# Optimization experiments

Measured on AMD Instinct MI355X. Metric: run time of the kernel, lower is better.

The kernel has to match this reference:

```python
import jax, jax.numpy as jnp
import numpy as np

FP16_HUGE = 65504.0  # large additive mask constant (fp16-max style, as in AF2 torch ports)

B, N, T = 1, 384, 4
CQ, CT = 128, 64      # query (pair) channels, template pair channels
H = 4                 # num heads
D = CT // H           # per-head key/value dim = 16 (AF2: key_dim=value_dim=64 split over 4 heads)


def setup_inputs() -> dict:
    key = jax.random.key(0)
    ks = jax.random.split(key, 8)
    inp = {
        "query_embedding": jax.random.normal(ks[0], (B, N, N, CQ), jnp.float32),
        "template_pair_representation": jax.random.normal(ks[1], (B, T, N, N, CT), jnp.float32),
        "template_mask": jnp.ones((B, T), jnp.float32),
        # attention params (gating=False for template pointwise attention in AF2)
        "query_w": jax.random.normal(ks[2], (H, CQ, D), jnp.float32) * (CQ ** -0.5),
        "key_w": jax.random.normal(ks[3], (H, CT, D), jnp.float32) * (CT ** -0.5),
        "value_w": jax.random.normal(ks[4], (H, CT, D), jnp.float32) * (CT ** -0.5),
        "output_w": jax.random.normal(ks[5], (H, D, CQ), jnp.float32) * ((H * D) ** -0.5),
        "output_b": jnp.zeros((CQ,), jnp.float32),
    }
    return inp


def reference(query_embedding, template_pair_representation, template_mask,
              query_w, key_w, value_w, output_w, output_b):
    b, n, _, cq = query_embedding.shape
    t = template_mask.shape[-1]
    d = query_w.shape[-1]

    # [b, n*n, 1, cq]: each (i,j) pair position attends over templates
    flat_q = query_embedding.reshape(b, n * n, 1, cq)
    # [b, t, n, n, ct] -> [b, n, n, t, ct] -> [b, n*n, t, ct]
    flat_t = jnp.transpose(template_pair_representation, (0, 2, 3, 1, 4)).reshape(b, n * n, t, -1)

    # additive bias over key axis: 0 where mask=1, -FP16_HUGE where mask=0; [b,1,1,1,t]
    bias = FP16_HUGE * (template_mask[:, None, None, None, :] - 1.0)

    q = jnp.einsum('bpic,hcd->bphid', flat_q, query_w) * (d ** -0.5)  # [b,p,h,1,d]
    k = jnp.einsum('bptc,hcd->bphtd', flat_t, key_w)                  # [b,p,h,t,d]
    v = jnp.einsum('bptc,hcd->bphtd', flat_t, value_w)

    logits = jnp.einsum('bphid,bphtd->bphit', q, k) + bias            # [b,p,h,1,t]
    weights = jax.nn.softmax(logits, axis=-1)
    wv = jnp.einsum('bphit,bphtd->bphid', weights, v)                 # [b,p,h,1,d]
    out = jnp.einsum('bphid,hdc->bpic', wv, output_w) + output_b      # [b,p,1,cq]

    embedding = out.reshape(b, n, n, cq)
    tmask = (jnp.sum(template_mask.reshape(b, -1), axis=1) > 0.0).astype(embedding.dtype)
    return embedding * tmask[:, None, None, None]
```

## Files before the change

kernel.cpp:

```cpp
#include <hip/hip_runtime.h>
#include <hip/hip_bf16.h>

typedef __attribute__((ext_vector_type(8))) short bf16x8;
typedef __attribute__((ext_vector_type(4))) float f32x4;
typedef unsigned int u32;
typedef unsigned short u16;

#define NPOS 147456
#define NTILES 9216
#define NBLK 768
#define ITERS 12

__device__ inline u16 bfc(float f) {
  union { __hip_bfloat16 h; u16 s; } u;
  u.h = __float2bfloat16(f);
  return u.s;
}

__global__ void prep_kernel(const float* __restrict__ wq, const float* __restrict__ wk,
                            const float* __restrict__ wv, const float* __restrict__ wo,
                            u16* __restrict__ wsf) {
  int gid = blockIdx.x * 256 + threadIdx.x;
  int idx, which;
  if (gid < 8192)       { idx = gid;         which = 0; }
  else if (gid < 12288) { idx = gid - 8192;  which = 1; }
  else if (gid < 16384) { idx = gid - 12288; which = 2; }
  else                  { idx = gid - 16384; which = 3; }
  int fragid = idx >> 9, lane = (idx >> 3) & 63, e = idx & 7;
  int l15 = lane & 15, g = lane >> 4;
  float v;
  if (which == 0) {
    int n = fragid >> 2, kc = fragid & 3;
    int c = kc * 32 + g * 8 + e;
    v = wq[n * 2048 + c * 16 + l15] * 0.25f;
  } else if (which == 1) {
    int n = fragid >> 1, kc = fragid & 1;
    int c = kc * 32 + g * 8 + e;
    v = wk[n * 1024 + c * 16 + l15];
  } else if (which == 2) {
    int n = fragid >> 1, kc = fragid & 1;
    int c = kc * 32 + g * 8 + e;
    v = wv[n * 1024 + c * 16 + l15];
  } else {
    int n8 = fragid >> 1, kc = fragid & 1;
    int hd = kc * 32 + g * 8 + e;
    v = wo[(hd >> 4) * 2048 + (hd & 15) * 128 + n8 * 16 + l15];
  }
  wsf[gid] = bfc(v);
}

#define WQF(n, kc)  ((((n) * 4 + (kc))) * 64)
#define WKF(n, kc)  ((16 + (n) * 2 + (kc)) * 64)
#define WVF(n, kc)  ((24 + (n) * 2 + (kc)) * 64)
#define WOF(n8, kc) ((32 + (n8) * 2 + (kc)) * 64)

typedef const __attribute__((address_space(1))) u32 gas_u32;
typedef __attribute__((address_space(3))) u32 las_u32;

__global__ __launch_bounds__(256) void tpa_kernel(
    const float* __restrict__ qe, const float* __restrict__ tpr,
    const float* __restrict__ tmk_p, const float* __restrict__ ob,
    const u16* __restrict__ wsf, float* __restrict__ out)
{
  __shared__ int4 inbuf4[2][1536];
  __shared__ u32 wvsh32[512];
  char* const inb0 = (char*)inbuf4[0];
  char* const inb1 = (char*)inbuf4[1];
  char* const wvsh = (char*)wvsh32;

  const int tid = threadIdx.x;
  const int wid = tid >> 6;
  const int lane = tid & 63;
  const int l15 = lane & 15, g = lane >> 4;
  const int swz = (l15 & 7) << 4;
  const int h = wid;

  const char* dmab[6]; int dmstr[6];
  #pragma unroll
  for (int j = 0; j < 6; ++j) {
    int k = wid + 4 * j, m = k * 64 + lane;
    if (m < 512) {
      int pos = m >> 5, inner = ((m & 31) * 16) ^ ((pos & 7) << 4);
      dmab[j] = (const char*)qe + (size_t)pos * 512 + inner; dmstr[j] = 512;
    } else {
      int m2 = m - 512, t = m2 >> 8, pos = (m2 >> 4) & 15;
      int inner = ((m2 & 15) * 16) ^ ((pos & 7) << 4);
      dmab[j] = (const char*)tpr + ((size_t)t * NPOS + pos) * 256 + inner; dmstr[j] = 256;
    }
  }

#define STAGE(DST, P)                                                          \
  { _Pragma("unroll") for (int j = 0; j < 6; ++j) {                            \
      const char* s_ = dmab[j] + (size_t)(P) * dmstr[j];                       \
      char* d_ = (DST) + (wid + 4 * j) * 1024;                                 \
      __builtin_amdgcn_global_load_lds((gas_u32*)s_, (las_u32*)d_, 16, 0, 0); } }

  STAGE(inb0, blockIdx.x * 16)

  const bf16x8* wf = (const bf16x8*)wsf;
  bf16x8 wqf[4], wkf[2], wvf[2], wof[2][2];
  #pragma unroll
  for (int kc = 0; kc < 4; ++kc) wqf[kc] = wf[WQF(h, kc) + lane];
  #pragma unroll
  for (int kc = 0; kc < 2; ++kc) {
    wkf[kc] = wf[WKF(h, kc) + lane];
    wvf[kc] = wf[WVF(h, kc) + lane];
    wof[0][kc] = wf[WOF(2 * h + 0, kc) + lane];
    wof[1][kc] = wf[WOF(2 * h + 1, kc) + lane];
  }

  const float m0 = tmk_p[0], m1 = tmk_p[1], m2 = tmk_p[2], m3 = tmk_p[3];
  const float biasv[4] = {65504.0f * (m0 - 1.0f), 65504.0f * (m1 - 1.0f),
                          65504.0f * (m2 - 1.0f), 65504.0f * (m3 - 1.0f)};
  const float tmk = (m0 + m1 + m2 + m3 > 0.0f) ? 1.0f : 0.0f;

  f32x4 obf[2];
  {
    const f32x4* obase = reinterpret_cast<const f32x4*>(ob);
    #pragma unroll
    for (int j = 0; j < 2; ++j) {
      const f32x4 o = obase[(2 * h + j) * 4 + g];
      #pragma unroll
      for (int r = 0; r < 4; ++r) obf[j][r] = o[r] * tmk;
    }
  }

  STAGE(inb1, (blockIdx.x + NBLK) * 16)

#define BODY(IT, CB)                                                           \
{                                                                              \
  const int p0 = (blockIdx.x + (IT) * NBLK) * 16;                              \
  __builtin_amdgcn_sched_barrier(0);                                           \
  asm volatile("s_waitcnt vmcnt(6)" ::: "memory");                             \
  __builtin_amdgcn_s_barrier();                                                \
  __builtin_amdgcn_sched_barrier(0);                                           \
  const char* qrow = (CB) + l15 * 512;                                         \
  f32x4 qT = (f32x4){0.f, 0.f, 0.f, 0.f};                                      \
  _Pragma("unroll")                                                            \
  for (int kc = 0; kc < 4; ++kc) {                                             \
    const int cb = kc * 128 + g * 32;                                          \
    f32x4 lo = *(const f32x4*)(qrow + ((cb) ^ swz));                           \
    f32x4 hi = *(const f32x4*)(qrow + ((cb + 16) ^ swz));                      \
    bf16x8 aq;                                                                 \
    _Pragma("unroll")                                                          \
    for (int e = 0; e < 4; ++e) { aq[e] = (short)bfc(lo[e]); aq[e + 4] = (short)bfc(hi[e]); } \
    qT = __builtin_amdgcn_mfma_f32_16x16x32_bf16(wqf[kc], aq, qT, 0, 0, 0);    \
  }                                                                            \
  float ssum = 0.f;                                                            \
  f32x4 wvT = (f32x4){0.f, 0.f, 0.f, 0.f};                                     \
  _Pragma("unroll")                                                            \
  for (int t = 0; t < 4; ++t) {                                                \
    const char* trow = (CB) + 8192 + t * 4096 + l15 * 256;                     \
    bf16x8 at0, at1;                                                           \
    { f32x4 lo = *(const f32x4*)(trow + ((g * 32) ^ swz));                     \
      f32x4 hi = *(const f32x4*)(trow + ((g * 32 + 16) ^ swz));                \
      _Pragma("unroll")                                                        \
      for (int e = 0; e < 4; ++e) { at0[e] = (short)bfc(lo[e]); at0[e + 4] = (short)bfc(hi[e]); } } \
    { f32x4 lo = *(const f32x4*)(trow + ((128 + g * 32) ^ swz));               \
      f32x4 hi = *(const f32x4*)(trow + ((128 + g * 32 + 16) ^ swz));          \
      _Pragma("unroll")                                                        \
      for (int e = 0; e < 4; ++e) { at1[e] = (short)bfc(lo[e]); at1[e + 4] = (short)bfc(hi[e]); } } \
    f32x4 kT = (f32x4){0.f, 0.f, 0.f, 0.f};                                    \
    f32x4 vT = (f32x4){0.f, 0.f, 0.f, 0.f};                                    \
    kT = __builtin_amdgcn_mfma_f32_16x16x32_bf16(wkf[0], at0, kT, 0, 0, 0);    \
    kT = __builtin_amdgcn_mfma_f32_16x16x32_bf16(wkf[1], at1, kT, 0, 0, 0);    \
    vT = __builtin_amdgcn_mfma_f32_16x16x32_bf16(wvf[0], at0, vT, 0, 0, 0);    \
    vT = __builtin_amdgcn_mfma_f32_16x16x32_bf16(wvf[1], at1, vT, 0, 0, 0);    \
    float lg = qT[0] * kT[0] + qT[1] * kT[1] + qT[2] * kT[2] + qT[3] * kT[3];  \
    lg += __shfl_xor(lg, 16);                                                  \
    lg += __shfl_xor(lg, 32);                                                  \
    const float w = __expf(lg + biasv[t]);                                     \
    ssum += w;                                                                 \
    _Pragma("unroll")                                                          \
    for (int r = 0; r < 4; ++r) wvT[r] += w * vT[r];                           \
  }                                                                            \
  { const float inv = tmk / fmaxf(ssum, 1e-30f);                               \
    u32 pk0 = (u32)bfc(wvT[0] * inv) | ((u32)bfc(wvT[1] * inv) << 16);         \
    u32 pk1 = (u32)bfc(wvT[2] * inv) | ((u32)bfc(wvT[3] * inv) << 16);         \
    const int hb = h * 32 + g * 8;                                             \
    *(u32*)(wvsh + ((l15 * 128 + hb) ^ swz))     = pk0;                        \
    *(u32*)(wvsh + ((l15 * 128 + hb + 4) ^ swz)) = pk1; }                      \
  __builtin_amdgcn_sched_barrier(0);                                           \
  asm volatile("s_waitcnt lgkmcnt(0)" ::: "memory");                           \
  __builtin_amdgcn_s_barrier();                                                \
  __builtin_amdgcn_sched_barrier(0);                                           \
  bf16x8 bwv0 = *(const bf16x8*)(wvsh + ((l15 * 128 + g * 16)      ^ swz));    \
  bf16x8 bwv1 = *(const bf16x8*)(wvsh + ((l15 * 128 + 64 + g * 16) ^ swz));    \
  _Pragma("unroll")                                                            \
  for (int j = 0; j < 2; ++j) {                                                \
    f32x4 acc = (f32x4){0.f, 0.f, 0.f, 0.f};                                   \
    acc = __builtin_amdgcn_mfma_f32_16x16x32_bf16(wof[j][0], bwv0, acc, 0, 0, 0); \
    acc = __builtin_amdgcn_mfma_f32_16x16x32_bf16(wof[j][1], bwv1, acc, 0, 0, 0); \
    f32x4 res;                                                                 \
    _Pragma("unroll")                                                          \
    for (int r = 0; r < 4; ++r) res[r] = acc[r] + obf[j][r];                   \
    *(f32x4*)(out + (size_t)(p0 + l15) * 128 + (2 * h + j) * 16 + g * 4) = res; \
  }                                                                            \
  __builtin_amdgcn_sched_barrier(0);                                           \
  { const int sit = ((IT) + 2 < ITERS) ? (IT) + 2 : (IT);                      \
    STAGE(CB, (blockIdx.x + sit * NBLK) * 16) }                                \
}

  for (int ith = 0; ith < ITERS / 2; ++ith) {
    BODY(2 * ith,     inb0)
    BODY(2 * ith + 1, inb1)
  }
}

extern "C" void kernel_launch(void* const* d_in, const int* in_sizes, int n_in,
                              void* d_out, int out_size, void* d_ws, size_t ws_size,
                              hipStream_t stream) {
  const float* qe  = (const float*)d_in[0];
  const float* tpr = (const float*)d_in[1];
  const float* tmk = (const float*)d_in[2];
  const float* wq  = (const float*)d_in[3];
  const float* wk  = (const float*)d_in[4];
  const float* wv  = (const float*)d_in[5];
  const float* wo  = (const float*)d_in[6];
  const float* ob  = (const float*)d_in[7];
  float* out = (float*)d_out;
  u16* wsf = (u16*)d_ws;

  prep_kernel<<<96, 256, 0, stream>>>(wq, wk, wv, wo, wsf);
  tpa_kernel<<<NBLK, 256, 0, stream>>>(qe, tpr, tmk, ob, wsf, out);
}
```

Measured before the change: 64.44 us.

## Load query rows straight to registers and issue template DMA earlier

Query-embedding rows are now loaded from global memory straight into registers, one iteration ahead, instead of going through the LDS DMA staging buffer. Only template-pair data is staged via global_load_lds, so the double buffer shrinks and the vmcnt wait thresholds are recomputed for the new load counts. The next-tile stage and query prefetch are issued right after the second barrier, before the output MFMAs and stores, to overlap more. A launch-bounds occupancy hint of 2 blocks is added, which trades register headroom for the extra live query registers against potential spilling.

```diff
diff --git a/kernel.cpp b/kernel.cpp
--- a/kernel.cpp
+++ b/kernel.cpp
@@ -57,12 +57,15 @@
 typedef const __attribute__((address_space(1))) u32 gas_u32;
 typedef __attribute__((address_space(3))) u32 las_u32;
 
-__global__ __launch_bounds__(256) void tpa_kernel(
+#define STR2_(x) #x
+#define WAITVM(n) asm volatile("s_waitcnt vmcnt(" STR2_(n) ")" ::: "memory")
+
+__global__ __launch_bounds__(256, 2) void tpa_kernel(
     const float* __restrict__ qe, const float* __restrict__ tpr,
     const float* __restrict__ tmk_p, const float* __restrict__ ob,
     const u16* __restrict__ wsf, float* __restrict__ out)
 {
-  __shared__ int4 inbuf4[2][1536];
+  __shared__ int4 inbuf4[2][1024];
   __shared__ u32 wvsh32[512];
   char* const inb0 = (char*)inbuf4[0];
   char* const inb1 = (char*)inbuf4[1];
@@ -75,27 +78,28 @@
   const int swz = (l15 & 7) << 4;
   const int h = wid;
 
-  const char* dmab[6]; int dmstr[6];
+  const char* dmab[4];
   #pragma unroll
-  for (int j = 0; j < 6; ++j) {
-    int k = wid + 4 * j, m = k * 64 + lane;
-    if (m < 512) {
-      int pos = m >> 5, inner = ((m & 31) * 16) ^ ((pos & 7) << 4);
-      dmab[j] = (const char*)qe + (size_t)pos * 512 + inner; dmstr[j] = 512;
-    } else {
-      int m2 = m - 512, t = m2 >> 8, pos = (m2 >> 4) & 15;
-      int inner = ((m2 & 15) * 16) ^ ((pos & 7) << 4);
-      dmab[j] = (const char*)tpr + ((size_t)t * NPOS + pos) * 256 + inner; dmstr[j] = 256;
-    }
+  for (int j = 0; j < 4; ++j) {
+    int m = (wid * 4 + j) * 64 + lane;
+    int t = m >> 8, pos = (m >> 4) & 15, c16 = m & 15;
+    int inner = (c16 * 16) ^ ((pos & 7) << 4);
+    dmab[j] = (const char*)tpr + ((size_t)t * NPOS + pos) * 256 + inner;
   }
 
 #define STAGE(DST, P)                                                          \
-  { _Pragma("unroll") for (int j = 0; j < 6; ++j) {                            \
-      const char* s_ = dmab[j] + (size_t)(P) * dmstr[j];                       \
-      char* d_ = (DST) + (wid + 4 * j) * 1024;                                 \
+  { _Pragma("unroll") for (int j = 0; j < 4; ++j) {                            \
+      const char* s_ = dmab[j] + (size_t)(P) * 256;                            \
+      char* d_ = (DST) + (wid * 4 + j) * 1024;                                 \
       __builtin_amdgcn_global_load_lds((gas_u32*)s_, (las_u32*)d_, 16, 0, 0); } }
 
-  STAGE(inb0, blockIdx.x * 16)
+#define LOADQ(P)                                                               \
+  { const f32x4* qb = reinterpret_cast<const f32x4*>(qe) + ((P) + l15) * 32 + g * 2; \
+    _Pragma("unroll")                                                          \
+    for (int kc = 0; kc < 4; ++kc) {                                           \
+      qv[kc * 2 + 0] = qb[kc * 8 + 0];                                         \
+      qv[kc * 2 + 1] = qb[kc * 8 + 1];                                         \
+    } }
 
   const bf16x8* wf = (const bf16x8*)wsf;
   bf16x8 wqf[4], wkf[2], wvf[2], wof[2][2];
@@ -125,32 +129,36 @@
     }
   }
 
+  f32x4 qv[8];
+  LOADQ(blockIdx.x * 16)
+  __builtin_amdgcn_sched_barrier(0);
+  STAGE(inb0, blockIdx.x * 16)
   STAGE(inb1, (blockIdx.x + NBLK) * 16)
-
-#define BODY(IT, CB)                                                           \
+  __builtin_amdgcn_sched_barrier(0);
+
+#define BODY(IT, CB, WN)                                                       \
 {                                                                              \
   const int p0 = (blockIdx.x + (IT) * NBLK) * 16;                              \
   __builtin_amdgcn_sched_barrier(0);                                           \
-  asm volatile("s_waitcnt vmcnt(6)" ::: "memory");                             \
+  WAITVM(WN);                                                                  \
   __builtin_amdgcn_s_barrier();                                                \
   __builtin_amdgcn_sched_barrier(0);                                           \
-  const char* qrow = (CB) + l15 * 512;                                         \
   f32x4 qT = (f32x4){0.f, 0.f, 0.f, 0.f};                                      \
   _Pragma("unroll")                                                            \
   for (int kc = 0; kc < 4; ++kc) {                                             \
-    const int cb = kc * 128 + g * 32;                                          \
-    f32x4 lo = *(const f32x4*)(qrow + ((cb) ^ swz));                           \
-    f32x4 hi = *(const f32x4*)(qrow + ((cb + 16) ^ swz));                      \
     bf16x8 aq;                                                                 \
     _Pragma("unroll")                                                          \
-    for (int e = 0; e < 4; ++e) { aq[e] = (short)bfc(lo[e]); aq[e + 4] = (short)bfc(hi[e]); } \
+    for (int e = 0; e < 4; ++e) {                                              \
+      aq[e]     = (short)bfc(qv[kc * 2 + 0][e]);                               \
+      aq[e + 4] = (short)bfc(qv[kc * 2 + 1][e]);                               \
+    }                                                                          \
     qT = __builtin_amdgcn_mfma_f32_16x16x32_bf16(wqf[kc], aq, qT, 0, 0, 0);    \
   }                                                                            \
   float ssum = 0.f;                                                            \
   f32x4 wvT = (f32x4){0.f, 0.f, 0.f, 0.f};                                     \
   _Pragma("unroll")                                                            \
   for (int t = 0; t < 4; ++t) {                                                \
-    const char* trow = (CB) + 8192 + t * 4096 + l15 * 256;                     \
+    const char* trow = (CB) + t * 4096 + l15 * 256;                            \
     bf16x8 at0, at1;                                                           \
     { f32x4 lo = *(const f32x4*)(trow + ((g * 32) ^ swz));                     \
       f32x4 hi = *(const f32x4*)(trow + ((g * 32 + 16) ^ swz));                \
@@ -182,7 +190,13 @@
     *(u32*)(wvsh + ((l15 * 128 + hb + 4) ^ swz)) = pk1; }                      \
   __builtin_amdgcn_sched_barrier(0);                                           \
   asm volatile("s_waitcnt lgkmcnt(0)" ::: "memory");                           \
-  __builtin_amdgcn_s_barrier();                                                \
+  __builtin_amdgcn_s_barrier();                \
+  __builtin_amdgcn_sched_barrier(0);                                           \
+  { const int nqp = ((IT) + 1 < ITERS) ? (blockIdx.x + ((IT) + 1) * NBLK) * 16 : p0; \
+    LOADQ(nqp) }                                                               \
+  __builtin_amdgcn_sched_barrier(0);                                           \
+  { const int sit = ((IT) + 2 < ITERS) ? (IT) + 2 : (IT);                      \
+    STAGE(CB, (blockIdx.x + sit * NBLK) * 16) }                                \
   __builtin_amdgcn_sched_barrier(0);                                           \
   bf16x8 bwv0 = *(const bf16x8*)(wvsh + ((l15 * 128 + g * 16)      ^ swz));    \
   bf16x8 bwv1 = *(const bf16x8*)(wvsh + ((l15 * 128 + 64 + g * 16) ^ swz));    \
@@ -196,14 +210,13 @@
     for (int r = 0; r < 4; ++r) res[r] = acc[r] + obf[j][r];                   \
     *(f32x4*)(out + (size_t)(p0 + l15) * 128 + (2 * h + j) * 16 + g * 4) = res; \
   }                                                                            \
-  __builtin_amdgcn_sched_barrier(0);                                           \
-  { const int sit = ((IT) + 2 < ITERS) ? (IT) + 2 : (IT);                      \
-    STAGE(CB, (blockIdx.x + sit * NBLK) * 16) }                                \
-}
-
-  for (int ith = 0; ith < ITERS / 2; ++ith) {
-    BODY(2 * ith,     inb0)
-    BODY(2 * ith + 1, inb1)
+}
+
+  BODY(0, inb0, 4)
+  BODY(1, inb1, 14)
+  for (int ith = 1; ith < ITERS / 2; ++ith) {
+    BODY(2 * ith,     inb0, 14)
+    BODY(2 * ith + 1, inb1, 14)
   }
 }
 
@@ -214,13 +227,13 @@
   const float* tpr = (const float*)d_in[1];
   const float* tmk = (const float*)d_in[2];
   const float* wq  = (const float*)d_in[3];
+  const float* wv_ = (const float*)d_in[5];
   const float* wk  = (const float*)d_in[4];
-  const float* wv  = (const float*)d_in[5];
   const float* wo  = (const float*)d_in[6];
   const float* ob  = (const float*)d_in[7];
   float* out = (float*)d_out;
   u16* wsf = (u16*)d_ws;
 
-  prep_kernel<<<96, 256, 0, stream>>>(wq, wk, wv, wo, wsf);
+  prep_kernel<<<96, 256, 0, stream>>>(wq, wk, wv_, wo, wsf);
   tpa_kernel<<<NBLK, 256, 0, stream>>>(qe, tpr, tmk, ob, wsf, out);
 }
```

New measurement: 79.31 us. 1.23x slower.

## Split staging into half buffers and double block count for occupancy

Applied to the files above, without the earlier changes.

Replaces the two full 24KB double buffers with a single query buffer plus two template-half buffers, cutting LDS per block roughly in half. Prefetch of the next tile's query and first template half is issued mid-iteration, and the second half after the output stores. The grid grows to 1536 blocks with 6 iterations each, so more blocks can be resident per CU. The cost is more barriers per iteration and a shallower prefetch, which can expose more load latency within each block.

```diff
diff --git a/kernel.cpp b/kernel.cpp
--- a/kernel.cpp
+++ b/kernel.cpp
@@ -8,8 +8,8 @@
 
 #define NPOS 147456
 #define NTILES 9216
-#define NBLK 768
-#define ITERS 12
+#define NBLK 1536
+#define ITERS 6
 
 __device__ inline u16 bfc(float f) {
   union { __hip_bfloat16 h; u16 s; } u;
@@ -57,15 +57,24 @@
 typedef const __attribute__((address_space(1))) u32 gas_u32;
 typedef __attribute__((address_space(3))) u32 las_u32;
 
+#define STR2_(x) #x
+#define WAITVM(n) asm volatile("s_waitcnt vmcnt(" STR2_(n) ")" ::: "memory")
+#define SBAR      __builtin_amdgcn_s_barrier()
+#define SCHB      __builtin_amdgcn_sched_barrier(0)
+#define WAITLGKM  asm volatile("s_waitcnt lgkmcnt(0)" ::: "memory")
+
 __global__ __launch_bounds__(256) void tpa_kernel(
     const float* __restrict__ qe, const float* __restrict__ tpr,
     const float* __restrict__ tmk_p, const float* __restrict__ ob,
     const u16* __restrict__ wsf, float* __restrict__ out)
 {
-  __shared__ int4 inbuf4[2][1536];
+  __shared__ int4 qls4[512];
+  __shared__ int4 thA4[512];
+  __shared__ int4 thB4[512];
   __shared__ u32 wvsh32[512];
-  char* const inb0 = (char*)inbuf4[0];
-  char* const inb1 = (char*)inbuf4[1];
+  char* const qls  = (char*)qls4;
+  char* const thA  = (char*)thA4;
+  char* const thB  = (char*)thB4;
   char* const wvsh = (char*)wvsh32;
 
   const int tid = threadIdx.x;
@@ -75,27 +84,35 @@
   const int swz = (l15 & 7) << 4;
   const int h = wid;
 
-  const char* dmab[6]; int dmstr[6];
-  #pragma unroll
-  for (int j = 0; j < 6; ++j) {
-    int k = wid + 4 * j, m = k * 64 + lane;
-    if (m < 512) {
-      int pos = m >> 5, inner = ((m & 31) * 16) ^ ((pos & 7) << 4);
-      dmab[j] = (const char*)qe + (size_t)pos * 512 + inner; dmstr[j] = 512;
-    } else {
-      int m2 = m - 512, t = m2 >> 8, pos = (m2 >> 4) & 15;
-      int inner = ((m2 & 15) * 16) ^ ((pos & 7) << 4);
-      dmab[j] = (const char*)tpr + ((size_t)t * NPOS + pos) * 256 + inner; dmstr[j] = 256;
+  const char* qdb[2];
+  #pragma unroll
+  for (int j = 0; j < 2; ++j) {
+    int m = (wid * 2 + j) * 64 + lane;
+    int pos = m >> 5, c16 = m & 31;
+    qdb[j] = (const char*)qe + (size_t)pos * 512 + ((c16 * 16) ^ ((pos & 7) << 4));
+  }
+  const char* tdb[2][2];
+  #pragma unroll
+  for (int hf = 0; hf < 2; ++hf)
+    #pragma unroll
+    for (int j = 0; j < 2; ++j) {
+      int m = (wid * 2 + j) * 64 + lane;
+      int t = hf * 2 + (m >> 8), pos = (m >> 4) & 15, c16 = m & 15;
+      tdb[hf][j] = (const char*)tpr + ((size_t)t * NPOS + pos) * 256 +
+                   ((c16 * 16) ^ ((pos & 7) << 4));
     }
-  }
-
-#define STAGE(DST, P)                                                          \
-  { _Pragma("unroll") for (int j = 0; j < 6; ++j) {                            \
-      const char* s_ = dmab[j] + (size_t)(P) * dmstr[j];                       \
-      char* d_ = (DST) + (wid + 4 * j) * 1024;                                 \
+
+#define STAGE_Q(P)                                                             \
+  { _Pragma("unroll") for (int j = 0; j < 2; ++j) {                            \
+      const char* s_ = qdb[j] + (size_t)(P) * 512;                             \
+      char* d_ = qls + (wid * 2 + j) * 1024;                                   \
       __builtin_amdgcn_global_load_lds((gas_u32*)s_, (las_u32*)d_, 16, 0, 0); } }
 
-  STAGE(inb0, blockIdx.x * 16)
+#define STAGE_T(HF, DST, P)                                                    \
+  { _Pragma("unroll") for (int j = 0; j < 2; ++j) {                            \
+      const char* s_ = tdb[HF][j] + (size_t)(P) * 256;                         \
+      char* d_ = (DST) + (wid * 2 + j) * 1024;                                 \
+      __builtin_amdgcn_global_load_lds((gas_u32*)s_, (las_u32*)d_, 16, 0, 0); } }
 
   const bf16x8* wf = (const bf16x8*)wsf;
   bf16x8 wqf[4], wkf[2], wvf[2], wof[2][2];
@@ -125,39 +142,20 @@
     }
   }
 
-  STAGE(inb1, (blockIdx.x + NBLK) * 16)
-
-#define BODY(IT, CB)                                                           \
-{                                                                              \
-  const int p0 = (blockIdx.x + (IT) * NBLK) * 16;                              \
-  __builtin_amdgcn_sched_barrier(0);                                           \
-  asm volatile("s_waitcnt vmcnt(6)" ::: "memory");                             \
-  __builtin_amdgcn_s_barrier();                                                \
-  __builtin_amdgcn_sched_barrier(0);                                           \
-  const char* qrow = (CB) + l15 * 512;                                         \
-  f32x4 qT = (f32x4){0.f, 0.f, 0.f, 0.f};                                      \
-  _Pragma("unroll")                                                            \
-  for (int kc = 0; kc < 4; ++kc) {                                             \
-    const int cb = kc * 128 + g * 32;                                          \
-    f32x4 lo = *(const f32x4*)(qrow + ((cb) ^ swz));                           \
-    f32x4 hi = *(const f32x4*)(qrow + ((cb + 16) ^ swz));                      \
-    bf16x8 aq;                                                                 \
-    _Pragma("unroll")                                                          \
-    for (int e = 0; e < 4; ++e) { aq[e] = (short)bfc(lo[e]); aq[e + 4] = (short)bfc(hi[e]); } \
-    qT = __builtin_amdgcn_mfma_f32_16x16x32_bf16(wqf[kc], aq, qT, 0, 0, 0);    \
-  }                                                                            \
-  float ssum = 0.f;                                                            \
-  f32x4 wvT = (f32x4){0.f, 0.f, 0.f, 0.f};                                     \
-  _Pragma("unroll")                                                            \
-  for (int t = 0; t < 4; ++t) {                                                \
-    const char* trow = (CB) + 8192 + t * 4096 + l15 * 256;                     \
-    bf16x8 at0, at1;                                                           \
-    { f32x4 lo = *(const f32x4*)(trow + ((g * 32) ^ swz));                     \
-      f32x4 hi = *(const f32x4*)(trow + ((g * 32 + 16) ^ swz));                \
+  SCHB;
+  STAGE_Q(blockIdx.x * 16)
+  STAGE_T(0, thA, blockIdx.x * 16)
+  STAGE_T(1, thB, blockIdx.x * 16)
+  SCHB;
+
+#define TSTEP(TROW, BIAS)                                                      \
+  { bf16x8 at0, at1;                                                           \
+    { f32x4 lo = *(const f32x4*)((TROW) + ((g * 32) ^ swz));                   \
+      f32x4 hi = *(const f32x4*)((TROW) + ((g * 32 + 16) ^ swz));              \
       _Pragma("unroll")                                                        \
       for (int e = 0; e < 4; ++e) { at0[e] = (short)bfc(lo[e]); at0[e + 4] = (short)bfc(hi[e]); } } \
-    { f32x4 lo = *(const f32x4*)(trow + ((128 + g * 32) ^ swz));               \
-      f32x4 hi = *(const f32x4*)(trow + ((128 + g * 32 + 16) ^ swz));          \
+    { f32x4 lo = *(const f32x4*)((TROW) + ((128 + g * 32) ^ swz));             \
+      f32x4 hi = *(const f32x4*)((TROW) + ((128 + g * 32 + 16) ^ swz));        \
       _Pragma("unroll")                                                        \
       for (int e = 0; e < 4; ++e) { at1[e] = (short)bfc(lo[e]); at1[e + 4] = (short)bfc(hi[e]); } } \
     f32x4 kT = (f32x4){0.f, 0.f, 0.f, 0.f};                                    \
@@ -169,41 +167,71 @@
     float lg = qT[0] * kT[0] + qT[1] * kT[1] + qT[2] * kT[2] + qT[3] * kT[3];  \
     lg += __shfl_xor(lg, 16);                                                  \
     lg += __shfl_xor(lg, 32);                                                  \
-    const float w = __expf(lg + biasv[t]);                                     \
+    const float w = __expf(lg + (BIAS));                                       \
     ssum += w;                                                                 \
     _Pragma("unroll")                                                          \
-    for (int r = 0; r < 4; ++r) wvT[r] += w * vT[r];                           \
-  }                                                                            \
+    for (int r = 0; r < 4; ++r) wvT[r] += w * vT[r]; }
+
+#define BODY(IT, WNA)                                                          \
+{                                                                              \
+  const int it_ = (IT);                                                        \
+  const int p0 = (blockIdx.x + it_ * NBLK) * 16;                               \
+  const int np0 = (blockIdx.x + ((it_ + 1 < ITERS) ? it_ + 1 : it_) * NBLK) * 16; \
+                                                    \
+  SCHB; WAITVM(WNA); SBAR; SCHB;                                               \
+  f32x4 qT = (f32x4){0.f, 0.f, 0.f, 0.f};                                      \
+  { const char* qrow = qls + l15 * 512;                                        \
+    _Pragma("unroll")                                                          \
+    for (int kc = 0; kc < 4; ++kc) {                                           \
+      const int cb = kc * 128 + g * 32;                                        \
+      f32x4 lo = *(const f32x4*)(qrow + ((cb) ^ swz));                         \
+      f32x4 hi = *(const f32x4*)(qrow + ((cb + 16) ^ swz));                    \
+      bf16x8 aq;                                                               \
+      _Pragma("unroll")                                                        \
+      for (int e = 0; e < 4; ++e) { aq[e] = (short)bfc(lo[e]); aq[e + 4] = (short)bfc(hi[e]); } \
+      qT = __builtin_amdgcn_mfma_f32_16x16x32_bf16(wqf[kc], aq, qT, 0, 0, 0);  \
+    } }                                                                        \
+  float ssum = 0.f;                                                            \
+  f32x4 wvT = (f32x4){0.f, 0.f, 0.f, 0.f};                                     \
+  TSTEP(thA + 0 * 4096 + l15 * 256, biasv[0])                                  \
+  TSTEP(thA + 1 * 4096 + l15 * 256, biasv[1])                                  \
+                                 \
+  SCHB; WAITLGKM; SBAR; SCHB;                                                  \
+  STAGE_Q(np0)                                                                 \
+  STAGE_T(0, thA, np0)                                                         \
+                                                        \
+  SCHB; WAITVM(4); SBAR; SCHB;                                                 \
+  TSTEP(thB + 0 * 4096 + l15 * 256, biasv[2])                                  \
+  TSTEP(thB + 1 * 4096 + l15 * 256, biasv[3])                                  \
   { const float inv = tmk / fmaxf(ssum, 1e-30f);                               \
     u32 pk0 = (u32)bfc(wvT[0] * inv) | ((u32)bfc(wvT[1] * inv) << 16);         \
     u32 pk1 = (u32)bfc(wvT[2] * inv) | ((u32)bfc(wvT[3] * inv) << 16);         \
     const int hb = h * 32 + g * 8;                                             \
     *(u32*)(wvsh + ((l15 * 128 + hb) ^ swz))     = pk0;                        \
     *(u32*)(wvsh + ((l15 * 128 + hb + 4) ^ swz)) = pk1; }                      \
-  __builtin_amdgcn_sched_barrier(0);                                           \
-  asm volatile("s_waitcnt lgkmcnt(0)" ::: "memory");                           \
-  __builtin_amdgcn_s_barrier();                                                \
-  __builtin_amdgcn_sched_barrier(0);                                           \
-  bf16x8 bwv0 = *(const bf16x8*)(wvsh + ((l15 * 128 + g * 16)      ^ swz));    \
-  bf16x8 bwv1 = *(const bf16x8*)(wvsh + ((l15 * 128 + 64 + g * 16) ^ swz));    \
-  _Pragma("unroll")                                                            \
-  for (int j = 0; j < 2; ++j) {                                                \
-    f32x4 acc = (f32x4){0.f, 0.f, 0.f, 0.f};                                   \
-    acc = __builtin_amdgcn_mfma_f32_16x16x32_bf16(wof[j][0], bwv0, acc, 0, 0, 0); \
-    acc = __builtin_amdgcn_mfma_f32_16x16x32_bf16(wof[j][1], bwv1, acc, 0, 0, 0); \
-    f32x4 res;                                                                 \
+                                             \
+  SCHB; WAITLGKM; SBAR; SCHB;                                                  \
+  { bf16x8 bwv0 = *(const bf16x8*)(wvsh + ((l15 * 128 + g * 16)      ^ swz));  \
+    bf16x8 bwv1 = *(const bf16x8*)(wvsh + ((l15 * 128 + 64 + g * 16) ^ swz));  \
     _Pragma("unroll")                                                          \
-    for (int r = 0; r < 4; ++r) res[r] = acc[r] + obf[j][r];                   \
-    *(f32x4*)(out + (size_t)(p0 + l15) * 128 + (2 * h + j) * 16 + g * 4) = res; \
-  }                                                                            \
-  __builtin_amdgcn_sched_barrier(0);                                           \
-  { const int sit = ((IT) + 2 < ITERS) ? (IT) + 2 : (IT);                      \
-    STAGE(CB, (blockIdx.x + sit * NBLK) * 16) }                                \
-}
-
-  for (int ith = 0; ith < ITERS / 2; ++ith) {
-    BODY(2 * ith,     inb0)
-    BODY(2 * ith + 1, inb1)
+    for (int j = 0; j < 2; ++j) {                                              \
+      f32x4 acc = (f32x4){0.f, 0.f, 0.f, 0.f};                                 \
+      acc = __builtin_amdgcn_mfma_f32_16x16x32_bf16(wof[j][0], bwv0, acc, 0, 0, 0); \
+      acc = __builtin_amdgcn_mfma_f32_16x16x32_bf16(wof[j][1], bwv1, acc, 0, 0, 0); \
+      f32x4 res;                                                               \
+      _Pragma("unroll")                                                        \
+      for (int r = 0; r < 4; ++r) res[r] = acc[r] + obf[j][r];                 \
+      *(f32x4*)(out + (size_t)(p0 + l15) * 128 + (2 * h + j) * 16 + g * 4) = res; \
+    } }                                                                        \
+  SCHB;                                                                        \
+  STAGE_T(1, thB, np0)                                                         \
+  SCHB;                                                                        \
+}
+
+  BODY(0, 2)
+  #pragma unroll 1
+  for (int it = 1; it < ITERS; ++it) {
+    BODY(it, 4)
   }
 }
 
```

After: 61.53 us. 1.05x faster.
